# Kernel optimization log

Hardware: AMD Instinct MI355X
Metric: run time of the kernel (lower is better)

## Reference

```python
import jax, jax.numpy as jnp
import numpy as np

B, LQ, LS, S = 64, 64, 512, 512
NEG = -1e6


def mask_for_lengths(lengths, max_len, mask_right=True):
    pos = jnp.arange(max_len)
    if mask_right:
        m = pos[None, :] >= lengths[:, None]
    else:
        m = pos[None, :] < lengths[:, None]
    return jnp.where(m, jnp.float32(NEG), jnp.float32(0.0))


def setup_inputs() -> dict:
    key = jax.random.key(0)
    ks = jax.random.split(key, 12)
    f = lambda k, shp: jax.random.normal(k, shp, jnp.float32)
    sc = np.float32(1.0 / np.sqrt(S))
    return {
        "encoded_question": f(ks[0], (B, LQ, S)),
        "encoded_support": f(ks[1], (B, LS, S)),
        "question_length": jax.random.randint(ks[2], (B,), 1, LQ + 1),
        "support_length": jax.random.randint(ks[3], (B,), LS // 2, LS + 1),
        "correct_start": jax.random.randint(ks[4], (B,), 0, LS),
        "answer2question": jnp.arange(B),
        "is_eval": 1,
        "W_qa": f(ks[5], (S, 1)) * sc,
        "W_qsi": f(ks[6], (S, S)) * sc,
        "b_qsi": jnp.zeros((S,), jnp.float32),
        "W_qs": f(ks[7], (2 * S, S)) * sc,
        "W_ss": f(ks[8], (S, 1)) * sc,
        "W_qei": f(ks[9], (S, S)) * sc,
        "b_qei": jnp.zeros((S,), jnp.float32),
        "W_qe": f(ks[10], (3 * S, S)) * sc,
        "W_es": f(ks[11], (S, 1)) * sc,
    }


def reference(encoded_question, encoded_support, question_length, support_length,
              correct_start, answer2question, is_eval,
              W_qa, W_qsi, b_qsi, W_qs, W_ss, W_qei, b_qei, W_qe, W_es):
    # question attention pooling
    att = jnp.einsum('bqd,do->bq', encoded_question, W_qa)
    att = att + mask_for_lengths(question_length, LQ)
    w = jax.nn.softmax(att, axis=1)                                   # [B,LQ]
    q_state = jnp.einsum('bqd,bq->bd', encoded_question, w)           # [B,S]

    # start scoring
    start_input = jnp.concatenate(
        [q_state[:, None, :] * encoded_support, encoded_support], axis=2)  # [B,LS,2S]
    q_start_inter = q_state @ W_qsi + b_qsi                           # [B,S]
    q_start_state = start_input @ W_qs + q_start_inter[:, None, :]    # [B,LS,S]
    support_mask = mask_for_lengths(support_length, LS)
    start_scores = jnp.einsum('bld,do->bl', jax.nn.relu(q_start_state), W_ss)
    start_scores = start_scores + support_mask                        # [B,LS]
    predicted_start_pointer = jnp.argmax(start_scores, axis=1)        # [B]

    # eval path: start_pointer = predicted argmax
    start_pointer = predicted_start_pointer
    u_s = jnp.take_along_axis(encoded_support,
                              start_pointer[:, None, None], axis=1)[:, 0, :]  # [B,S]

    # end scoring
    end_input = jnp.concatenate(
        [encoded_support * u_s[:, None, :], start_input], axis=2)     # [B,LS,3S]
    q_end_inter = q_state @ W_qei + b_qei
    q_end_state = end_input @ W_qe + q_end_inter[:, None, :]          # [B,LS,S]
    end_scores = jnp.einsum('bld,do->bl', jax.nn.relu(q_end_state), W_es)
    end_scores = end_scores + support_mask
    # eval: mask positions left of start_pointer
    end_scores = end_scores + mask_for_lengths(start_pointer, LS, mask_right=False)
    predicted_end_pointer = jnp.argmax(end_scores, axis=1)

    return (start_scores, end_scores, predicted_start_pointer, predicted_end_pointer)
```

## Files before the change

kernel.cpp:

```cpp
#include <hip/hip_runtime.h>
#include <math.h>

constexpr int B_  = 64;
constexpr int LQ_ = 64;
constexpr int LS_ = 512;
constexpr int S_  = 512;
#define NEGV (-1e6f)
#define MARGIN 0.0625f

typedef __attribute__((ext_vector_type(8))) short bf16x8;
typedef __attribute__((ext_vector_type(4))) float f32x4;

__device__ inline unsigned short f2bf_rn(float x) {
    unsigned u = __builtin_bit_cast(unsigned, x);
    unsigned r = (u + 0x7FFFu + ((u >> 16) & 1u)) >> 16;
    return (unsigned short)r;
}

__global__ __launch_bounds__(512)
void qpool_inter_kernel(const float* __restrict__ eq, const int* __restrict__ qlen,
                        const float* __restrict__ W_qa,
                        const float* __restrict__ W_qsi, const float* __restrict__ b_qsi,
                        const float* __restrict__ W_qei, const float* __restrict__ b_qei,
                        float* __restrict__ q_state,
                        float* __restrict__ qsi, float* __restrict__ qei)
{
    int b = blockIdx.x;
    int which = blockIdx.y;
    const float* W  = which ? W_qei : W_qsi;
    const float* bi = which ? b_qei : b_qsi;
    float*       o  = which ? qei   : qsi;

    int t = threadIdx.x, lane = t & 63, w = t >> 6;
    __shared__ float att[LQ_], wsm[LQ_], qs[S_];
    __shared__ float red[8][S_];
    const float* eqb = eq + (size_t)b * LQ_ * S_;

    #pragma unroll
    for (int k = 0; k < 8; ++k) {
        int q = w + 8 * k;
        const float* row = eqb + q * S_;
        float s = 0.f;
        #pragma unroll
        for (int j = 0; j < 8; ++j)
            s = fmaf(row[lane + 64 * j], W_qa[lane + 64 * j], s);
        #pragma unroll
        for (int off = 32; off >= 1; off >>= 1)
            s += __shfl_xor(s, off);
        if (lane == 0) att[q] = s;
    }
    __syncthreads();

    if (w == 0) {
        int L = qlen[b];
        float v = att[lane] + ((lane < L) ? 0.f : NEGV);
        float m = v;
        #pragma unroll
        for (int off = 32; off >= 1; off >>= 1)
            m = fmaxf(m, __shfl_xor(m, off));
        float e = expf(v - m);
        float sum = e;
        #pragma unroll
        for (int off = 32; off >= 1; off >>= 1)
            sum += __shfl_xor(sum, off);
        wsm[lane] = e / sum;
    }
    __syncthreads();

    {
        float acc = 0.f;
        #pragma unroll 8
        for (int q = 0; q < LQ_; ++q)
            acc = fmaf(wsm[q], eqb[q * S_ + t], acc);
        qs[t] = acc;
        if (which == 0) q_state[b * S_ + t] = acc;
    }
    __syncthreads();

    {
        float z[8];
        #pragma unroll
        for (int k = 0; k < 8; ++k) z[k] = 0.f;
        const int d0 = w * 64;
        #pragma unroll 4
        for (int dd = 0; dd < 64; ++dd) {
            int d = d0 + dd;
            float q = qs[d];
            const float* row = W + (size_t)d * S_ + lane;
            #pragma unroll
            for (int k = 0; k < 8; ++k)
                z[k] = fmaf(q, row[k * 64], z[k]);
        }
        #pragma unroll
        for (int k = 0; k < 8; ++k) red[w][k * 64 + lane] = z[k];
    }
    __syncthreads();
    {
        float acc = bi[t];
        #pragma unroll
        for (int ww = 0; ww < 8; ++ww) acc += red[ww][t];
        o[b * S_ + t] = acc;
    }
}

__device__ inline int select_cands(const float* s_l, int t, int lane, int w,
                                   float* wred, int* wcnt, int* cand)
{
    float v = s_l[t];
    #pragma unroll
    for (int off = 32; off >= 1; off >>= 1)
        v = fmaxf(v, __shfl_xor(v, off));
    if (lane == 0) wred[w] = v;
    __syncthreads();
    float m = wred[0];
    #pragma unroll
    for (int k = 1; k < 8; ++k) m = fmaxf(m, wred[k]);
    float th = m - MARGIN;
    bool flag = s_l[t] >= th;
    unsigned long long bal = __ballot(flag);
    int rank = __popcll(bal & ((1ull << lane) - 1ull));
    if (lane == 0) wcnt[w] = (int)__popcll(bal);
    __syncthreads();
    int off = 0, total = 0;
    #pragma unroll
    for (int k = 0; k < 8; ++k) { if (k < w) off += wcnt[k]; total += wcnt[k]; }
    if (flag) { int pos = off + rank; if (pos < 8) cand[pos] = t; }
    __syncthreads();
    return total < 8 ? total : 8;
}

__global__ __launch_bounds__(512)
void prep_start_kernel(const float* __restrict__ W, const float* __restrict__ q_state,
                       short* __restrict__ Wc)
{
    int bid = blockIdx.x;
    int i = bid >> 6, b = bid & 63;
    int col = threadIdx.x;
    __shared__ float scq[32];
    if (col < 32) scq[col] = q_state[b * S_ + i * 32 + col];
    __syncthreads();

    unsigned short h[32];
    #pragma unroll
    for (int d = 0; d < 32; ++d) {
        int D = i * 32 + d;
        float v = fmaf(scq[d], W[(size_t)D * S_ + col], W[(size_t)(S_ + D) * S_ + col]);
        h[d] = f2bf_rn(v);
    }
    size_t base = (size_t)b * 262144 + (size_t)i * 16384 + (size_t)col * 8;
    #pragma unroll
    for (int kc = 0; kc < 4; ++kc) {
        uint4 H;
        H.x = h[kc*8+0] | ((unsigned)h[kc*8+1] << 16);
        H.y = h[kc*8+2] | ((unsigned)h[kc*8+3] << 16);
        H.z = h[kc*8+4] | ((unsigned)h[kc*8+5] << 16);
        H.w = h[kc*8+6] | ((unsigned)h[kc*8+7] << 16);
        *(uint4*)&Wc[base + kc * 4096] = H;
    }
}

__global__ __launch_bounds__(512)
void prep_end_kernel(const float* __restrict__ W, const float* __restrict__ q_state,
                     const float* __restrict__ es, const float* __restrict__ start_scores,
                     const float* __restrict__ part,
                     int* __restrict__ sp_ws, float* __restrict__ pred_start,
                     short* __restrict__ Wc)
{
    int bid = blockIdx.x;
    int i = bid >> 6, b = bid & 63;
    int t = threadIdx.x, lane = t & 63, w = t >> 6;
    __shared__ float s_l[S_];
    __shared__ float wred[8];
    __shared__ int wcnt[8], cand[8];
    __shared__ float scq[32], scu[32];
    __shared__ int best_sh;

    s_l[t] = start_scores[b * S_ + t];
    __syncthreads();
    int cnt = select_cands(s_l, t, lane, w, wred, wcnt, cand);

    if (t == 0) {
        int bi = cand[0];
        if (cnt > 1) {
            float bv = -INFINITY;
            for (int c = 0; c < cnt; ++c) {
                float e = part[b * 8 + c];
                if (e > bv) { bv = e; bi = cand[c]; }
            }
        }
        best_sh = bi;
        if (i == 0) { pred_start[b] = (float)bi; sp_ws[b] = bi; }
    }
    __syncthreads();
    int best = best_sh;

    if (t < 32) scq[t] = q_state[b * S_ + i * 32 + t];
    if (t >= 32 && t < 64)
        scu[t - 32] = es[((size_t)(b * LS_ + best)) * S_ + i * 32 + (t - 32)];
    __syncthreads();

    int col = t;
    unsigned short h[32];
    #pragma unroll
    for (int d = 0; d < 32; ++d) {
        int D = i * 32 + d;
        float v = fmaf(scu[d], W[(size_t)D * S_ + col],
                  fmaf(scq[d], W[(size_t)(S_ + D) * S_ + col],
                       W[(size_t)(2 * S_ + D) * S_ + col]));
        h[d] = f2bf_rn(v);
    }
    size_t base = (size_t)b * 262144 + (size_t)i * 16384 + (size_t)col * 8;
    #pragma unroll
    for (int kc = 0; kc < 4; ++kc) {
        uint4 H;
        H.x = h[kc*8+0] | ((unsigned)h[kc*8+1] << 16);
        H.y = h[kc*8+2] | ((unsigned)h[kc*8+3] << 16);
        H.z = h[kc*8+4] | ((unsigned)h[kc*8+5] << 16);
        H.w = h[kc*8+6] | ((unsigned)h[kc*8+7] << 16);
        *(uint4*)&Wc[base + kc * 4096] = H;
    }
}

template <bool END>
__global__ __launch_bounds__(512)
void score_kernel(const float* __restrict__ es, const short* __restrict__ Wc,
                  const float* __restrict__ inter, const float* __restrict__ Wsmall,
                  const int* __restrict__ slen, const int* __restrict__ sp,
                  float* __restrict__ out)
{
    const int t = threadIdx.x;
    const int lane = t & 63, wid = t >> 6;
    const int wr = wid >> 2, wc = wid & 3;
    const int l15 = lane & 15, l4 = lane >> 4;

    int lid = blockIdx.x;
    int xcd = lid & 7, slot = lid >> 3;
    int b  = xcd * 8 + (slot >> 2);
    int rc = slot & 3;

    __shared__ __attribute__((aligned(16))) short As[2][4096];
    __shared__ __attribute__((aligned(16))) short Bs[2][16384];
    __shared__ float int_l[S_], wsm_l[S_];
    __shared__ float sm_red[128][4];

    int_l[t] = inter[b * S_ + t];
    wsm_l[t] = Wsmall[t];

    const char* Bbase = (const char*)(Wc + (size_t)b * 262144);

    f32x4 acc[4][8];
    #pragma unroll
    for (int r = 0; r < 4; ++r)
        #pragma unroll
        for (int c = 0; c < 8; ++c)
            acc[r][c] = (f32x4){0.f, 0.f, 0.f, 0.f};

    const int arow = t >> 2, akc = t & 3;
    const float* aptr = es + ((size_t)(b * LS_ + rc * 128 + arow)) * S_ + akc * 8;

    auto buildA = [&](int buf, float4 a0, float4 a1) {
        uint4 HA;
        HA.x = f2bf_rn(a0.x) | ((unsigned)f2bf_rn(a0.y) << 16);
        HA.y = f2bf_rn(a0.z) | ((unsigned)f2bf_rn(a0.w) << 16);
        HA.z = f2bf_rn(a1.x) | ((unsigned)f2bf_rn(a1.y) << 16);
        HA.w = f2bf_rn(a1.z) | ((unsigned)f2bf_rn(a1.w) << 16);
        *(uint4*)&As[buf][akc * 1024 + arow * 8] = HA;
    };
    auto mfma_step = [&](int buf) {
        bf16x8 ah[4];
        #pragma unroll
        for (int r = 0; r < 4; ++r) {
            int rowp = wr * 64 + r * 16 + l15;
            ah[r] = *(const bf16x8*)&As[buf][l4 * 1024 + rowp * 8];
        }
        #pragma unroll
        for (int c = 0; c < 8; ++c) {
            int col = wc * 128 + c * 16 + l15;
            bf16x8 bh = *(const bf16x8*)&Bs[buf][l4 * 4096 + col * 8];
            #pragma unroll
            for (int r = 0; r < 4; ++r)
                acc[r][c] = __builtin_amdgcn_mfma_f32_16x16x32_bf16(ah[r], bh, acc[r][c], 0, 0, 0);
        }
    };

    uint4 P0, P1, P2, P3, Q0, Q1, Q2, Q3;
    {
        const char* gb = Bbase + t * 16;
        P0 = *(const uint4*)(gb);
        P1 = *(const uint4*)(gb + 8192);
        P2 = *(const uint4*)(gb + 16384);
        P3 = *(const uint4*)(gb + 24576);
        const char* gb1 = gb + 32768;
        Q0 = *(const uint4*)(gb1);
        Q1 = *(const uint4*)(gb1 + 8192);
        Q2 = *(const uint4*)(gb1 + 16384);
        Q3 = *(const uint4*)(gb1 + 24576);
    }
    float4 pa0 = *(const float4*)(aptr);
    float4 pa1 = *(const float4*)(aptr + 4);
    float4 qa0 = *(const float4*)(aptr + 32);
    float4 qa1 = *(const float4*)(aptr + 36);

    #pragma unroll 1
    for (int ii = 0; ii < 8; ++ii) {
        const int i = ii * 2;

        {
            char* lb = (char*)Bs[0] + t * 16;
            *(uint4*)(lb)         = P0;
            *(uint4*)(lb + 8192)  = P1;
            *(uint4*)(lb + 16384) = P2;
            *(uint4*)(lb + 24576) = P3;
        }
        buildA(0, pa0, pa1);
        if (i + 2 < 16) {
            const char* gb = Bbase + (size_t)(i + 2) * 32768 + t * 16;
            P0 = *(const uint4*)(gb);
            P1 = *(const uint4*)(gb + 8192);
            P2 = *(const uint4*)(gb + 16384);
            P3 = *(const uint4*)(gb + 24576);
            pa0 = *(const float4*)(aptr + (i + 2) * 32);
            pa1 = *(const float4*)(aptr + (i + 2) * 32 + 4);
        }
        asm volatile("s_waitcnt lgkmcnt(0)" ::: "memory");
        __builtin_amdgcn_s_barrier();
        mfma_step(0);

        {
            char* lb = (char*)Bs[1] + t * 16;
            *(uint4*)(lb)         = Q0;
            *(uint4*)(lb + 8192)  = Q1;
            *(uint4*)(lb + 16384) = Q2;
            *(uint4*)(lb + 24576) = Q3;
        }
        buildA(1, qa0, qa1);
        if (i + 3 < 16) {
            const char* gb = Bbase + (size_t)(i + 3) * 32768 + t * 16;
            Q0 = *(const uint4*)(gb);
            Q1 = *(const uint4*)(gb + 8192);
            Q2 = *(const uint4*)(gb + 16384);
            Q3 = *(const uint4*)(gb + 24576);
            qa0 = *(const float4*)(aptr + (i + 3) * 32);
            qa1 = *(const float4*)(aptr + (i + 3) * 32 + 4);
        }
        asm volatile("s_waitcnt lgkmcnt(0)" ::: "memory");
        __builtin_amdgcn_s_barrier();
        mfma_step(1);
    }

    #pragma unroll
    for (int r = 0; r < 4; ++r) {
        #pragma unroll
        for (int jj = 0; jj < 4; ++jj) {
            float pr = 0.f;
            #pragma unroll
            for (int c = 0; c < 8; ++c) {
                int col = wc * 128 + c * 16 + l15;
                float v = acc[r][c][jj] + int_l[col];
                v = fmaxf(v, 0.f);
                pr = fmaf(v, wsm_l[col], pr);
            }
            pr += __shfl_xor(pr, 1);
            pr += __shfl_xor(pr, 2);
            pr += __shfl_xor(pr, 4);
            pr += __shfl_xor(pr, 8);
            if (l15 == 0) sm_red[wr * 64 + r * 16 + l4 * 4 + jj][wc] = pr;
        }
    }
    __syncthreads();
    if (t < 128) {
        int l = rc * 128 + t;
        float s = sm_red[t][0] + sm_red[t][1] + sm_red[t][2] + sm_red[t][3];
        if (l >= slen[b]) s += NEGV;
        if (END) { if (l < sp[b]) s += NEGV; }
        out[b * LS_ + l] = s;
    }
}

template <bool END>
__global__ __launch_bounds__(512)
void rescue_kernel(const float* __restrict__ support, const float* __restrict__ q_state,
                   const int* __restrict__ sp, const float* __restrict__ Wbig,
                   const float* __restrict__ inter, const float* __restrict__ Wsmall,
                   const float* __restrict__ scores, float* __restrict__ part)
{
    int bid = blockIdx.x;
    int b = bid >> 3, cslot = bid & 7;
    int t = threadIdx.x, lane = t & 63, w = t >> 6;
    __shared__ float s_l[S_], qs_l[S_], us_l[S_], arow_sh[S_];
    __shared__ float red[8][S_];
    __shared__ float wred[8];
    __shared__ int wcnt[8], cand[8];

    s_l[t]  = scores[b * S_ + t];
    qs_l[t] = q_state[b * S_ + t];
    if (END) {
        int spv = sp[b];
        us_l[t] = support[((size_t)(b * LS_ + spv)) * S_ + t];
    }
    __syncthreads();

    int cnt = select_cands(s_l, t, lane, w, wred, wcnt, cand);
    if (cnt == 1 || cslot >= cnt) return;

    int ci = cand[cslot];
    arow_sh[t] = support[((size_t)(b * LS_ + ci)) * S_ + t];
    __syncthreads();

    const float* W1 = Wbig;
    const float* W2 = Wbig + (size_t)S_ * S_;
    const float* W3 = Wbig + (size_t)2 * S_ * S_;
    const int d0 = w * 64;

    float z[8];
    #pragma unroll
    for (int j = 0; j < 8; ++j) z[j] = 0.f;

    #pragma unroll 2
    for (int dd = 0; dd < 64; ++dd) {
        int d = d0 + dd;
        float a  = arow_sh[d];
        float qa = qs_l[d] * a;
        float ua = END ? us_l[d] * a : 0.f;
        const float* r1 = W1 + (size_t)d * S_ + lane;
        const float* r2 = W2 + (size_t)d * S_ + lane;
        const float* r3 = W3 + (size_t)d * S_ + lane;
        #pragma unroll
        for (int j = 0; j < 8; ++j) {
            if (END)
                z[j] = fmaf(ua, r1[64 * j], fmaf(qa, r2[64 * j], fmaf(a, r3[64 * j], z[j])));
            else
                z[j] = fmaf(qa, r1[64 * j], fmaf(a, r2[64 * j], z[j]));
        }
    }
    #pragma unroll
    for (int j = 0; j < 8; ++j) red[w][lane + 64 * j] = z[j];
    __syncthreads();

    float v = 0.f;
    #pragma unroll
    for (int ww = 0; ww < 8; ++ww) v += red[ww][t];
    float p = fmaxf(v + inter[b * S_ + t], 0.f) * Wsmall[t];
    #pragma unroll
    for (int off = 32; off >= 1; off >>= 1)
        p += __shfl_xor(p, off);
    if (lane == 0) wred[w] = p;
    __syncthreads();
    if (t == 0) {
        float e = ((wred[0] + wred[1]) + (wred[2] + wred[3])) +
                  ((wred[4] + wred[5]) + (wred[6] + wred[7]));
        part[b * 8 + cslot] = e;
    }
}

__global__ __launch_bounds__(512)
void finalize_end_kernel(const float* __restrict__ scores, const float* __restrict__ part,
                         float* __restrict__ pred)
{
    int b = blockIdx.x;
    int t = threadIdx.x, lane = t & 63, w = t >> 6;
    __shared__ float s_l[S_];
    __shared__ float wred[8];
    __shared__ int wcnt[8], cand[8];

    s_l[t] = scores[b * S_ + t];
    __syncthreads();
    int cnt = select_cands(s_l, t, lane, w, wred, wcnt, cand);

    if (t == 0) {
        int bi = cand[0];
        if (cnt > 1) {
            float bv = -INFINITY;
            for (int c = 0; c < cnt; ++c) {
                float e = part[b * 8 + c];
                if (e > bv) { bv = e; bi = cand[c]; }
            }
        }
        pred[b] = (float)bi;
    }
}

extern "C" void kernel_launch(void* const* d_in, const int* in_sizes, int n_in,
                              void* d_out, int out_size, void* d_ws, size_t ws_size,
                              hipStream_t stream)
{
    const float* eq    = (const float*)d_in[0];
    const float* es    = (const float*)d_in[1];
    const int*   qlen  = (const int*)d_in[2];
    const int*   slen  = (const int*)d_in[3];
    const float* W_qa  = (const float*)d_in[7];
    const float* W_qsi = (const float*)d_in[8];
    const float* b_qsi = (const float*)d_in[9];
    const float* W_qs  = (const float*)d_in[10];
    const float* W_ss  = (const float*)d_in[11];
    const float* W_qei = (const float*)d_in[12];
    const float* b_qei = (const float*)d_in[13];
    const float* W_qe  = (const float*)d_in[14];
    const float* W_es  = (const float*)d_in[15];

    float* out          = (float*)d_out;
    float* start_scores = out;
    float* end_scores   = out + B_ * LS_;
    float* pred_start   = out + 2 * B_ * LS_;
    float* pred_end     = out + 2 * B_ * LS_ + B_;

    float* ws      = (float*)d_ws;
    float* q_state = ws;
    float* qsi     = ws + B_ * S_;
    float* qei     = ws + 2 * B_ * S_;
    float* part    = ws + 3 * B_ * S_;
    int*   sp_ws   = (int*)(ws + 3 * B_ * S_ + 512);
    short* Wc      = (short*)(ws + 3 * B_ * S_ + 1024);

    qpool_inter_kernel<<<dim3(B_, 2), 512, 0, stream>>>(
        eq, qlen, W_qa, W_qsi, b_qsi, W_qei, b_qei, q_state, qsi, qei);

    prep_start_kernel<<<1024, 512, 0, stream>>>(W_qs, q_state, Wc);
    score_kernel<false><<<256, 512, 0, stream>>>(es, Wc, qsi, W_ss, slen, nullptr, start_scores);
    rescue_kernel<false><<<B_ * 8, 512, 0, stream>>>(es, q_state, nullptr, W_qs, qsi, W_ss,
                                                     start_scores, part);

    prep_end_kernel<<<1024, 512, 0, stream>>>(W_qe, q_state, es, start_scores, part,
                                              sp_ws, pred_start, Wc);
    score_kernel<true><<<256, 512, 0, stream>>>(es, Wc, qei, W_es, slen, sp_ws, end_scores);
    rescue_kernel<true><<<B_ * 8, 512, 0, stream>>>(es, q_state, sp_ws, W_qe, qei, W_es,
                                                    end_scores, part);
    finalize_end_kernel<<<B_, 512, 0, stream>>>(end_scores, part, pred_end);
}
```

Measured before the change: 162.9 us.

## Pre-convert support to bf16 tiles and stream GEMM operands via direct global-to-LDS loads

Adds a prep kernel that converts encoded_support to bf16 once, already laid out in the MFMA tile order, so both score kernels reuse it instead of each converting fp32 in registers. The score kernel main loop now uses global_load_lds to copy A and B tiles straight into a triple-buffered LDS ring with vmcnt-based waits, removing the register staging and LDS store instructions. The cost is an extra kernel launch, an extra bf16 copy of the support tensor in workspace, and more LDS per block.

```diff
diff --git a/kernel.cpp b/kernel.cpp
--- a/kernel.cpp
+++ b/kernel.cpp
@@ -103,6 +103,30 @@
     }
 }
 
+__global__ __launch_bounds__(512)
+void prep_es_kernel(const float* __restrict__ es, short* __restrict__ Aprep)
+{
+    int bid = blockIdx.x;
+    int t = threadIdx.x;
+    const float* slab = es + (size_t)bid * 128 * S_;
+    short* dst = Aprep + (size_t)bid * 65536;
+
+    #pragma unroll 4
+    for (int q = 0; q < 32; ++q) {
+        int g = q * 2048 + t * 4;
+        int row = g >> 9;
+        int k   = g & 511;
+        int i   = k >> 5;
+        int kc  = (k >> 3) & 3;
+        int e   = k & 7;
+        float4 v = *(const float4*)(slab + g);
+        uint2 P;
+        P.x = f2bf_rn(v.x) | ((unsigned)f2bf_rn(v.y) << 16);
+        P.y = f2bf_rn(v.z) | ((unsigned)f2bf_rn(v.w) << 16);
+        *(uint2*)&dst[i * 4096 + (kc * 128 + row) * 8 + e] = P;
+    }
+}
+
 __device__ inline int select_cands(const float* s_l, int t, int lane, int w,
                                    float* wred, int* wcnt, int* cand)
 {
@@ -223,7 +247,7 @@
 
 template <bool END>
 __global__ __launch_bounds__(512)
-void score_kernel(const float* __restrict__ es, const short* __restrict__ Wc,
+void score_kernel(const short* __restrict__ Aprep, const short* __restrict__ Wc,
                   const float* __restrict__ inter, const float* __restrict__ Wsmall,
                   const int* __restrict__ slen, const int* __restrict__ sp,
                   float* __restrict__ out)
@@ -238,14 +262,15 @@
     int b  = xcd * 8 + (slot >> 2);
     int rc = slot & 3;
 
-    __shared__ __attribute__((aligned(16))) short As[2][4096];
-    __shared__ __attribute__((aligned(16))) short Bs[2][16384];
+    __shared__ __attribute__((aligned(16))) short As3[3][4096];
+    __shared__ __attribute__((aligned(16))) short Bs3[3][16384];
     __shared__ float int_l[S_], wsm_l[S_];
     __shared__ float sm_red[128][4];
 
     int_l[t] = inter[b * S_ + t];
     wsm_l[t] = Wsmall[t];
 
+    const char* Abase = (const char*)(Aprep + ((size_t)(b * 4 + rc)) * 65536);
     const char* Bbase = (const char*)(Wc + (size_t)b * 262144);
 
     f32x4 acc[4][8];
@@ -255,97 +280,49 @@
         for (int c = 0; c < 8; ++c)
             acc[r][c] = (f32x4){0.f, 0.f, 0.f, 0.f};
 
-    const int arow = t >> 2, akc = t & 3;
-    const float* aptr = es + ((size_t)(b * LS_ + rc * 128 + arow)) * S_ + akc * 8;
-
-    auto buildA = [&](int buf, float4 a0, float4 a1) {
-        uint4 HA;
-        HA.x = f2bf_rn(a0.x) | ((unsigned)f2bf_rn(a0.y) << 16);
-        HA.y = f2bf_rn(a0.z) | ((unsigned)f2bf_rn(a0.w) << 16);
-        HA.z = f2bf_rn(a1.x) | ((unsigned)f2bf_rn(a1.y) << 16);
-        HA.w = f2bf_rn(a1.z) | ((unsigned)f2bf_rn(a1.w) << 16);
-        *(uint4*)&As[buf][akc * 1024 + arow * 8] = HA;
+    auto stage = [&](int i, int buf) {
+        const char* ga = Abase + (size_t)i * 8192 + t * 16;
+        char* la = (char*)As3[buf] + t * 16;
+        __builtin_amdgcn_global_load_lds(
+            (const __attribute__((address_space(1))) void*)ga,
+            (__attribute__((address_space(3))) void*)la, 16, 0, 0);
+        const char* gb = Bbase + (size_t)i * 32768 + t * 16;
+        char* lb = (char*)Bs3[buf] + t * 16;
+        #pragma unroll
+        for (int q = 0; q < 4; ++q)
+            __builtin_amdgcn_global_load_lds(
+                (const __attribute__((address_space(1))) void*)(gb + q * 8192),
+                (__attribute__((address_space(3))) void*)(lb + q * 8192), 16, 0, 0);
     };
-    auto mfma_step = [&](int buf) {
+
+    stage(0, 0);
+    stage(1, 1);
+
+    for (int i = 0; i < 16; ++i) {
+        const int buf = i % 3;
+        if (i + 2 < 16) stage(i + 2, (i + 2) % 3);
+
+        if (i + 2 < 16)      asm volatile("s_waitcnt vmcnt(10)" ::: "memory");
+        else if (i + 1 < 16) asm volatile("s_waitcnt vmcnt(5)" ::: "memory");
+        else                 asm volatile("s_waitcnt vmcnt(0)" ::: "memory");
+        __builtin_amdgcn_s_barrier();
+
         bf16x8 ah[4];
         #pragma unroll
         for (int r = 0; r < 4; ++r) {
             int rowp = wr * 64 + r * 16 + l15;
-            ah[r] = *(const bf16x8*)&As[buf][l4 * 1024 + rowp * 8];
+            ah[r] = *(const bf16x8*)&As3[buf][l4 * 1024 + rowp * 8];
         }
         #pragma unroll
         for (int c = 0; c < 8; ++c) {
             int col = wc * 128 + c * 16 + l15;
-            bf16x8 bh = *(const bf16x8*)&Bs[buf][l4 * 4096 + col * 8];
+            bf16x8 bh = *(const bf16x8*)&Bs3[buf][l4 * 4096 + col * 8];
             #pragma unroll
             for (int r = 0; r < 4; ++r)
                 acc[r][c] = __builtin_amdgcn_mfma_f32_16x16x32_bf16(ah[r], bh, acc[r][c], 0, 0, 0);
         }
-    };
-
-    uint4 P0, P1, P2, P3, Q0, Q1, Q2, Q3;
-    {
-        const char* gb = Bbase + t * 16;
-        P0 = *(const uint4*)(gb);
-        P1 = *(const uint4*)(gb + 8192);
-        P2 = *(const uint4*)(gb + 16384);
-        P3 = *(const uint4*)(gb + 24576);
-        const char* gb1 = gb + 32768;
-        Q0 = *(const uint4*)(gb1);
-        Q1 = *(const uint4*)(gb1 + 8192);
-        Q2 = *(const uint4*)(gb1 + 16384);
-        Q3 = *(const uint4*)(gb1 + 24576);
-    }
-    float4 pa0 = *(const float4*)(aptr);
-    float4 pa1 = *(const float4*)(aptr + 4);
-    float4 qa0 = *(const float4*)(aptr + 32);
-    float4 qa1 = *(const float4*)(aptr + 36);
-
-    #pragma unroll 1
-    for (int ii = 0; ii < 8; ++ii) {
-        const int i = ii * 2;
-
-        {
-            char* lb = (char*)Bs[0] + t * 16;
-            *(uint4*)(lb)         = P0;
-            *(uint4*)(lb + 8192)  = P1;
-            *(uint4*)(lb + 16384) = P2;
-            *(uint4*)(lb + 24576) = P3;
-        }
-        buildA(0, pa0, pa1);
-        if (i + 2 < 16) {
-            const char* gb = Bbase + (size_t)(i + 2) * 32768 + t * 16;
-            P0 = *(const uint4*)(gb);
-            P1 = *(const uint4*)(gb + 8192);
-            P2 = *(const uint4*)(gb + 16384);
-            P3 = *(const uint4*)(gb + 24576);
-            pa0 = *(const float4*)(aptr + (i + 2) * 32);
-            pa1 = *(const float4*)(aptr + (i + 2) * 32 + 4);
-        }
         asm volatile("s_waitcnt lgkmcnt(0)" ::: "memory");
         __builtin_amdgcn_s_barrier();
-        mfma_step(0);
-
-        {
-            char* lb = (char*)Bs[1] + t * 16;
-            *(uint4*)(lb)         = Q0;
-            *(uint4*)(lb + 8192)  = Q1;
-            *(uint4*)(lb + 16384) = Q2;
-            *(uint4*)(lb + 24576) = Q3;
-        }
-        buildA(1, qa0, qa1);
-        if (i + 3 < 16) {
-            const char* gb = Bbase + (size_t)(i + 3) * 32768 + t * 16;
-            Q0 = *(const uint4*)(gb);
-            Q1 = *(const uint4*)(gb + 8192);
-            Q2 = *(const uint4*)(gb + 16384);
-            Q3 = *(const uint4*)(gb + 24576);
-            qa0 = *(const float4*)(aptr + (i + 3) * 32);
-            qa1 = *(const float4*)(aptr + (i + 3) * 32 + 4);
-        }
-        asm volatile("s_waitcnt lgkmcnt(0)" ::: "memory");
-        __builtin_amdgcn_s_barrier();
-        mfma_step(1);
     }
 
     #pragma unroll
@@ -511,18 +488,20 @@
     float* part    = ws + 3 * B_ * S_;
     int*   sp_ws   = (int*)(ws + 3 * B_ * S_ + 512);
     short* Wc      = (short*)(ws + 3 * B_ * S_ + 1024);
+    short* Aprep   = Wc + (size_t)B_ * 16 * 16384;
 
     qpool_inter_kernel<<<dim3(B_, 2), 512, 0, stream>>>(
         eq, qlen, W_qa, W_qsi, b_qsi, W_qei, b_qei, q_state, qsi, qei);
+    prep_es_kernel<<<B_ * 4, 512, 0, stream>>>(es, Aprep);
 
     prep_start_kernel<<<1024, 512, 0, stream>>>(W_qs, q_state, Wc);
-    score_kernel<false><<<256, 512, 0, stream>>>(es, Wc, qsi, W_ss, slen, nullptr, start_scores);
+    score_kernel<false><<<256, 512, 0, stream>>>(Aprep, Wc, qsi, W_ss, slen, nullptr, start_scores);
     rescue_kernel<false><<<B_ * 8, 512, 0, stream>>>(es, q_state, nullptr, W_qs, qsi, W_ss,
                                                      start_scores, part);
 
     prep_end_kernel<<<1024, 512, 0, stream>>>(W_qe, q_state, es, start_scores, part,
                                               sp_ws, pred_start, Wc);
-    score_kernel<true><<<256, 512, 0, stream>>>(es, Wc, qei, W_es, slen, sp_ws, end_scores);
+    score_kernel<true><<<256, 512, 0, stream>>>(Aprep, Wc, qei, W_es, slen, sp_ws, end_scores);
     rescue_kernel<true><<<B_ * 8, 512, 0, stream>>>(es, q_state, sp_ws, W_qe, qei, W_es,
                                                     end_scores, part);
     finalize_end_kernel<<<B_, 512, 0, stream>>>(end_scores, part, pred_end);
```

Result: slower. 189.3 us (+16.2%).
